# Optimization experiments

Hardware: AMD Instinct MI355X
Metric: run time of the kernel (lower is better)

## Reference

```python
import jax, jax.numpy as jnp
import numpy as np

B, S, D, H = 4, 2048, 1024, 16
HD = D // H  # head_dim = 64


def setup_inputs() -> dict:
    key = jax.random.key(0)
    k1, k2, k3 = jax.random.split(key, 3)
    x = jax.random.normal(k1, (B, S, D), dtype=jnp.float32)
    W_attn = jax.random.normal(k2, (D, 3 * D), dtype=jnp.float32) * (1.0 / np.sqrt(D))
    b_attn = jnp.zeros((3 * D,), dtype=jnp.float32)
    W_proj = jax.random.normal(k3, (D, D), dtype=jnp.float32) * (1.0 / np.sqrt(D))
    b_proj = jnp.zeros((D,), dtype=jnp.float32)
    return {"x": x, "W_attn": W_attn, "b_attn": b_attn, "W_proj": W_proj, "b_proj": b_proj}


def reference(x, W_attn, b_attn, W_proj, b_proj):
    bsz, seq_len, d = x.shape
    n_head = H
    head_dim = d // n_head
    qkv = x @ W_attn + b_attn                      # [B,S,3D]
    q, k, v = jnp.split(qkv, 3, axis=-1)           # each [B,S,D]
    # -> [B,H,S,hd]
    q = q.reshape(bsz, seq_len, n_head, head_dim).transpose(0, 2, 1, 3)
    k = k.reshape(bsz, seq_len, n_head, head_dim).transpose(0, 2, 1, 3)
    v = v.reshape(bsz, seq_len, n_head, head_dim).transpose(0, 2, 1, 3)
    scale = 1.0 / np.sqrt(head_dim).astype(np.float32)
    att = jnp.einsum("bhqd,bhkd->bhqk", q, k) * scale  # [B,H,S,S]
    causal = jnp.tril(jnp.ones((seq_len, seq_len), dtype=bool))
    att = jnp.where(causal[None, None], att, jnp.float32(-jnp.inf))
    att = jax.nn.softmax(att, axis=-1)
    y = jnp.einsum("bhqk,bhkd->bhqd", att, v)       # [B,H,S,hd]
    y = y.transpose(0, 2, 1, 3).reshape(bsz, seq_len, d)
    return y @ W_proj + b_proj
```

## Files before the change

kernel.cpp:

```cpp
#include <hip/hip_runtime.h>

typedef __attribute__((ext_vector_type(8))) short short8;
typedef __attribute__((ext_vector_type(8))) __bf16 bf16x8;
typedef __attribute__((ext_vector_type(2))) __bf16 bf16x2;
typedef __attribute__((ext_vector_type(4))) float f32x4;
typedef __attribute__((ext_vector_type(2))) unsigned int uint2v;

#define LOG2E 1.44269504088896340736f

__device__ __forceinline__ unsigned short f2b(float f) {
  unsigned u = __builtin_bit_cast(unsigned, f);
  u += 0x7fffu + ((u >> 16) & 1u);
  return (unsigned short)(u >> 16);
}
__device__ __forceinline__ float b2f(unsigned short s) {
  unsigned u = (unsigned)s << 16;
  return __builtin_bit_cast(float, u);
}
__device__ __forceinline__ bf16x8 asbf(short8 s) { return __builtin_bit_cast(bf16x8, s); }

__device__ __forceinline__ void gl_lds16(const void* g, void* l) {
  __builtin_amdgcn_global_load_lds(
      (const __attribute__((address_space(1))) void*)g,
      (__attribute__((address_space(3))) void*)l, 16, 0, 0);
}

__device__ __forceinline__ unsigned lds_a(const void* p) {
  return (unsigned)(size_t)(__attribute__((address_space(3))) const void*)p;
}

__device__ __forceinline__ unsigned pk_bf16(float a, float b) {
  bf16x2 v;
  v[0] = (__bf16)a;
  v[1] = (__bf16)b;
  return __builtin_bit_cast(unsigned, v);
}

__global__ void k_cvt_bf16(const float* __restrict__ x, unsigned short* __restrict__ o, int n) {
  int i = (blockIdx.x * 256 + threadIdx.x) * 4;
  if (i >= n) return;
  float4 v = *(const float4*)(x + i);
  ushort4 r;
  r.x = f2b(v.x); r.y = f2b(v.y); r.z = f2b(v.z); r.w = f2b(v.w);
  *(ushort4*)(o + i) = r;
}

__global__ void k_transpose_bf16(const float* __restrict__ W, unsigned short* __restrict__ Wt,
                                 int R, int C) {
  __shared__ float tile[64][65];
  const int tc = blockIdx.x, tr = blockIdx.y;
  const int r0 = tr * 64, c0 = tc * 64;
  for (int it = 0; it < 16; ++it) {
    int lin = it * 256 + threadIdx.x;
    int r = lin >> 6, c = lin & 63;
    tile[r][c] = W[(size_t)(r0 + r) * C + c0 + c];
  }
  __syncthreads();
  for (int it = 0; it < 16; ++it) {
    int lin = it * 256 + threadIdx.x;
    int orr = lin >> 6, oc = lin & 63;
    Wt[(size_t)(c0 + orr) * R + r0 + oc] = f2b(tile[oc][orr]);
  }
}

template <int BNW, bool OUT_BF16>
__global__ __launch_bounds__(512, 4)
void k_gemm256(const unsigned short* __restrict__ A, const unsigned short* __restrict__ Bt,
               const float* __restrict__ bias, void* __restrict__ Cp,
               int M, int N, int K) {
  constexpr int BN = BNW * 4;
  constexpr int NR = BNW / 16;
  __shared__ unsigned short lds[2][512 * 32];

  const int tid = threadIdx.x;
  const int wv = tid >> 6, lane = tid & 63;
  const int g = lane >> 4, l15 = lane & 15;
  const int wr = wv >> 2, wc = wv & 3;

  const int ntn = N / BN;
  const int nwg = gridDim.x;
  const int bid = blockIdx.x;
  const int cpx = nwg >> 3;
  const int swz = (bid & 7) * cpx + (bid >> 3);
  const int tm = swz / ntn, tn = swz % ntn;

  const unsigned short* Ab = A + (size_t)(tm * 256) * K;
  const unsigned short* Bb = Bt + (size_t)(tn * BN) * K;

  const int NT = K >> 5;

  auto As = [&](int buf) -> char* { return (char*)&lds[buf][0]; };
  auto Bs = [&](int buf) -> char* { return (char*)&lds[buf][256 * 32]; };

  auto stageA = [&](int buf, int t) {
#pragma unroll
    for (int it = 0; it < 2; ++it) {
      int cidx = it * 512 + tid;
      int row = cidx >> 2, c8 = cidx & 3;
      int sc = c8 ^ ((row >> 1) & 3);
      gl_lds16(Ab + (size_t)row * K + t * 32 + sc * 8, As(buf) + cidx * 16);
    }
  };
  auto stageB = [&](int buf, int t) {
#pragma unroll
    for (int it = 0; it < 2; ++it) {
      int cidx = it * 512 + tid;
      int row = cidx >> 2, c8 = cidx & 3;
      int sc = c8 ^ ((row >> 1) & 3);
      int grow = (row < BN) ? row : 0;
      gl_lds16(Bb + (size_t)grow * K + t * 32 + sc * 8, Bs(buf) + cidx * 16);
    }
  };

  auto rdA = [&](int buf, int ms) -> short8 {
    int row = wr * 128 + ms * 16 + l15;
    int ch = g ^ ((row >> 1) & 3);
    return *(const short8*)(As(buf) + row * 64 + ch * 16);
  };
  auto rdB = [&](int buf, int n) -> short8 {
    int row = wc * BNW + n * 16 + l15;
    int ch = g ^ ((row >> 1) & 3);
    return *(const short8*)(Bs(buf) + row * 64 + ch * 16);
  };

  f32x4 acc[8][NR] = {};

  stageA(0, 0);
  stageB(0, 0);
  stageB(1, 1);
  asm volatile("s_waitcnt vmcnt(2)" ::: "memory");
  __builtin_amdgcn_s_barrier();

  for (int t = 0; t < NT; ++t) {
    const int buf = t & 1, nbuf = buf ^ 1;
    short8 bfr[NR], a0, a1;

    if (t + 1 < NT) stageA(nbuf, t + 1);
#pragma unroll
    for (int n = 0; n < NR; ++n) bfr[n] = rdB(buf, n);
    a0 = rdA(buf, 0);
    a1 = rdA(buf, 1);
    asm volatile("s_waitcnt lgkmcnt(0)" ::: "memory");
    __builtin_amdgcn_sched_barrier(0);
    __builtin_amdgcn_s_barrier();
    __builtin_amdgcn_s_setprio(1);
#pragma unroll
    for (int n = 0; n < NR; ++n) {
      acc[0][n] = __builtin_amdgcn_mfma_f32_16x16x32_bf16(asbf(a0), asbf(bfr[n]), acc[0][n], 0, 0, 0);
      acc[1][n] = __builtin_amdgcn_mfma_f32_16x16x32_bf16(asbf(a1), asbf(bfr[n]), acc[1][n], 0, 0, 0);
    }
    a0 = rdA(buf, 2);
    a1 = rdA(buf, 3);
#pragma unroll
    for (int n = 0; n < NR; ++n) {
      acc[2][n] = __builtin_amdgcn_mfma_f32_16x16x32_bf16(asbf(a0), asbf(bfr[n]), acc[2][n], 0, 0, 0);
      acc[3][n] = __builtin_amdgcn_mfma_f32_16x16x32_bf16(asbf(a1), asbf(bfr[n]), acc[3][n], 0, 0, 0);
    }
    __builtin_amdgcn_s_setprio(0);

    if (t + 2 < NT) stageB(buf, t + 2);
    a0 = rdA(buf, 4);
    a1 = rdA(buf, 5);
    asm volatile("s_waitcnt lgkmcnt(0)" ::: "memory");
    __builtin_amdgcn_sched_barrier(0);
    __builtin_amdgcn_s_barrier();
    __builtin_amdgcn_s_setprio(1);
#pragma unroll
    for (int n = 0; n < NR; ++n) {
      acc[4][n] = __builtin_amdgcn_mfma_f32_16x16x32_bf16(asbf(a0), asbf(bfr[n]), acc[4][n], 0, 0, 0);
      acc[5][n] = __builtin_amdgcn_mfma_f32_16x16x32_bf16(asbf(a1), asbf(bfr[n]), acc[5][n], 0, 0, 0);
    }
    a0 = rdA(buf, 6);
    a1 = rdA(buf, 7);
#pragma unroll
    for (int n = 0; n < NR; ++n) {
      acc[6][n] = __builtin_amdgcn_mfma_f32_16x16x32_bf16(asbf(a0), asbf(bfr[n]), acc[6][n], 0, 0, 0);
      acc[7][n] = __builtin_amdgcn_mfma_f32_16x16x32_bf16(asbf(a1), asbf(bfr[n]), acc[7][n], 0, 0, 0);
    }
    __builtin_amdgcn_s_setprio(0);
    if (t + 2 < NT) asm volatile("s_waitcnt vmcnt(2)" ::: "memory");
    else            asm volatile("s_waitcnt vmcnt(0)" ::: "memory");
    __builtin_amdgcn_s_barrier();
  }

  const int crow0 = tm * 256 + wr * 128 + g * 4;
  const int ccol0 = tn * BN + wc * BNW + l15;
#pragma unroll
  for (int n = 0; n < NR; ++n) {
    int col = ccol0 + n * 16;
    float bv = bias[col];
#pragma unroll
    for (int mq = 0; mq < 8; ++mq)
#pragma unroll
      for (int j = 0; j < 4; ++j) {
        int row = crow0 + mq * 16 + j;
        float v = acc[mq][n][j] + bv;
        if constexpr (OUT_BF16)
          ((unsigned short*)Cp)[(size_t)row * N + col] = f2b(v);
        else
          ((float*)Cp)[(size_t)row * N + col] = v;
      }
  }
}

__global__ __launch_bounds__(512)
void k_attn(const unsigned short* __restrict__ qkv, unsigned short* __restrict__ y) {
  constexpr int SEQ = 2048, TD = 3072, DM = 1024;
  __shared__ unsigned short Kl[2][4096];
  __shared__ unsigned short Vl[2][4096];
  __shared__ unsigned short Pl[8][2048];

  const int f = blockIdx.x;
  const int wrk = (f & 7) * 32 + (f >> 3);
  const int bh = wrk >> 2, pr = wrk & 3;
  const int b = bh >> 4, h = bh & 15;
  const int tid = threadIdx.x;
  const int lane = tid & 63, w = tid >> 6;
  const int g = lane >> 4, l15 = lane & 15;

  const size_t base = (size_t)b * SEQ * TD + h * 64;
  const unsigned short* Kg0 = qkv + base + 1024;
  const unsigned short* Vg0 = qkv + base + 2048;

  short8 onesb;
#pragma unroll
  for (int i = 0; i < 8; ++i) onesb[i] = (short)0x3F80;

  auto stage = [&](int buf, int c) {
    const unsigned short* Kg = Kg0 + (size_t)(c * 64) * TD;
    const unsigned short* Vg = Vg0 + (size_t)(c * 64) * TD;
    const int j = tid;
    int r = j >> 3, cc = j & 7;
    int cck = cc ^ (r & 7);
    gl_lds16(Kg + (size_t)r * TD + cck * 8, (char*)Kl[buf] + j * 16);
    int kv = ((j >> 1) & 3) | (((j >> 5) & 1) << 2) | (((j >> 3) & 3) << 3) |
             (((j >> 6) & 1) << 5);
    int d0 = ((j >> 7) << 4) | ((j & 1) << 3);
    gl_lds16(Vg + (size_t)kv * TD + d0, (char*)Vl[buf] + j * 16);
  };

  char* pw = (char*)Pl + w * 4096;

  for (int half = 0; half < 2; ++half) {
    const int qt = half ? (7 - pr) : pr;
    const int q0 = qt * 256;
    const int qw = w * 32;

    short8 qf[2][2];
#pragma unroll
    for (int qg = 0; qg < 2; ++qg) {
      const unsigned short* qrow = qkv + base + (size_t)(q0 + qw + qg * 16 + l15) * TD;
#pragma unroll
      for (int kh = 0; kh < 2; ++kh) {
        short8 t = *(const short8*)(qrow + kh * 32 + g * 8);
#pragma unroll
        for (int i = 0; i < 8; ++i)
          t[i] = (short)f2b(b2f((unsigned short)t[i]) * (0.125f * LOG2E));
        qf[qg][kh] = t;
      }
    }

    f32x4 o[2][4] = {};
    f32x4 ol[2] = {};

    const int nch = 4 * (qt + 1);
    int cur = 0;
    stage(0, 0);
    for (int c = 0; c < nch; ++c) {
      if (c + 1 < nch) {
        stage(cur ^ 1, c + 1);
        asm volatile("s_waitcnt vmcnt(2)" ::: "memory");
      } else {
        asm volatile("s_waitcnt vmcnt(0)" ::: "memory");
      }
      __builtin_amdgcn_s_barrier();

      f32x4 sv[2][4];
      __builtin_amdgcn_s_setprio(1);
#pragma unroll
      for (int ff = 0; ff < 4; ++ff) {
        int kv = ff * 16 + l15;
        short8 kf0 = *(const short8*)((const char*)Kl[cur] + kv * 128 + ((g) ^ (kv & 7)) * 16);
        short8 kf1 = *(const short8*)((const char*)Kl[cur] + kv * 128 + ((4 + g) ^ (kv & 7)) * 16);
#pragma unroll
        for (int qg = 0; qg < 2; ++qg) {
          f32x4 s = {};
          s = __builtin_amdgcn_mfma_f32_16x16x32_bf16(asbf(kf0), asbf(qf[qg][0]), s, 0, 0, 0);
          s = __builtin_amdgcn_mfma_f32_16x16x32_bf16(asbf(kf1), asbf(qf[qg][1]), s, 0, 0, 0);
          sv[qg][ff] = s;
        }
      }
      __builtin_amdgcn_s_setprio(0);

      const int crel = c - 4 * qt;
      if (crel >= 0) {
#pragma unroll
        for (int qg = 0; qg < 2; ++qg)
#pragma unroll
          for (int ff = 0; ff < 4; ++ff)
#pragma unroll
            for (int r = 0; r < 4; ++r)
              if (crel * 64 + ff * 16 + g * 4 + r > qw + qg * 16 + l15)
                sv[qg][ff][r] = -128.f;
      }

#pragma unroll
      for (int qg = 0; qg < 2; ++qg)
#pragma unroll
        for (int ff = 0; ff < 4; ++ff) {
          float p0 = __builtin_amdgcn_exp2f(sv[qg][ff][0]);
          float p1 = __builtin_amdgcn_exp2f(sv[qg][ff][1]);
          float p2 = __builtin_amdgcn_exp2f(sv[qg][ff][2]);
          float p3 = __builtin_amdgcn_exp2f(sv[qg][ff][3]);
          unsigned w0 = pk_bf16(p0, p1);
          unsigned w1 = pk_bf16(p2, p3);
          unsigned long long pk = (unsigned long long)w0 | ((unsigned long long)w1 << 32);
          int off = qg * 2048 + ((l15 * 128 + ff * 32 + g * 8) ^ ((l15 & 7) << 4));
          *(unsigned long long*)(pw + off) = pk;
        }

      const unsigned vaddr = lds_a((const char*)Vl[cur] + g * 128 + l15 * 8);
#pragma unroll
      for (int kvh = 0; kvh < 2; ++kvh) {
        uint2v t0[4], t1[4];
#pragma unroll
        for (int n = 0; n < 4; ++n) {
          asm volatile("ds_read_b64_tr_b16 %0, %1 offset:%2"
                       : "=v"(t0[n]) : "v"(vaddr), "i"(n * 2048 + kvh * 1024));
          asm volatile("ds_read_b64_tr_b16 %0, %1 offset:%2"
                       : "=v"(t1[n]) : "v"(vaddr), "i"(n * 2048 + kvh * 1024 + 512));
        }
        asm volatile("s_waitcnt lgkmcnt(0)" ::: "memory");
        __builtin_amdgcn_sched_barrier(0);
        __builtin_amdgcn_s_setprio(1);
#pragma unroll
        for (int qg = 0; qg < 2; ++qg) {
          short8 pa = *(const short8*)(pw + qg * 2048 +
                                       ((l15 * 128 + kvh * 64 + g * 16) ^ ((l15 & 7) << 4)));
#pragma unroll
          for (int n = 0; n < 4; ++n) {
            union { uint2v u[2]; short8 s; } uu;
            uu.u[0] = t0[n]; uu.u[1] = t1[n];
            o[qg][n] = __builtin_amdgcn_mfma_f32_16x16x32_bf16(asbf(pa), asbf(uu.s),
                                                               o[qg][n], 0, 0, 0);
          }
          ol[qg] = __builtin_amdgcn_mfma_f32_16x16x32_bf16(asbf(pa), asbf(onesb),
                                                           ol[qg], 0, 0, 0);
        }
        __builtin_amdgcn_s_setprio(0);
      }

      __builtin_amdgcn_s_barrier();
      cur ^= 1;
    }

#pragma unroll
    for (int qg = 0; qg < 2; ++qg) {
      float lj[4];
#pragma unroll
      for (int j = 0; j < 4; ++j) lj[j] = 1.f / ol[qg][j];
#pragma unroll
      for (int n = 0; n < 4; ++n)
#pragma unroll
        for (int j = 0; j < 4; ++j) {
          int row = q0 + qw + qg * 16 + g * 4 + j;
          int col = h * 64 + n * 16 + l15;
          y[(size_t)(b * SEQ + row) * DM + col] = f2b(o[qg][n][j] * lj[j]);
        }
    }
  }
}

extern "C" void kernel_launch(void* const* d_in, const int* in_sizes, int n_in,
                              void* d_out, int out_size, void* d_ws, size_t ws_size,
                              hipStream_t stream) {
  const float* x = (const float*)d_in[0];
  const float* W_attn = (const float*)d_in[1];
  const float* b_attn = (const float*)d_in[2];
  const float* W_proj = (const float*)d_in[3];
  const float* b_proj = (const float*)d_in[4];
  float* out = (float*)d_out;

  const int B = 4, S = 2048, D = 1024;
  const int M = B * S;
  const int TD = 3 * D;

  char* ws = (char*)d_ws;
  unsigned short* qkvb = (unsigned short*)ws;
  unsigned short* xb = (unsigned short*)(ws + (size_t)M * TD * 2);
  unsigned short* Wat = (unsigned short*)(ws + (size_t)M * TD * 2 + (size_t)M * D * 2);
  unsigned short* Wpt = Wat + (size_t)TD * D;

  k_cvt_bf16<<<(M * D) / 1024, 256, 0, stream>>>(x, xb, M * D);
  k_transpose_bf16<<<dim3(TD / 64, D / 64), 256, 0, stream>>>(W_attn, Wat, D, TD);
  k_transpose_bf16<<<dim3(D / 64, D / 64), 256, 0, stream>>>(W_proj, Wpt, D, D);

  k_gemm256<48, true><<<(M / 256) * (TD / 192), 512, 0, stream>>>(xb, Wat, b_attn, qkvb, M, TD, D);
  k_attn<<<256, 512, 0, stream>>>(qkvb, xb);
  k_gemm256<32, false><<<(M / 256) * (D / 128), 512, 0, stream>>>(xb, Wpt, b_proj, out, M, D, D);
}
```

Before: 191.2 us.

## Fuse prep kernels, unify GEMM to 256x128 tiles, double attention KV chunk

Merges the x-to-bf16 conversion and both weight transposes into one prep launch, which removes two kernel launches. Replaces the templated GEMM with a single 256x128 tile variant for both projections, so the QKV GEMM moves from 192-wide to 128-wide N tiles and one B load per stage. Doubles the attention KV chunk from 64 to 128 keys, which halves the number of barriers and staging rounds per query tile at the cost of twice the LDS use and more registers for scores. The smaller QKV tile raises the block count but reduces reuse per block, and the larger LDS footprint may lower attention occupancy.

```diff
diff --git a/kernel.cpp b/kernel.cpp
--- a/kernel.cpp
+++ b/kernel.cpp
@@ -36,44 +36,65 @@
   return __builtin_bit_cast(unsigned, v);
 }
 
-__global__ void k_cvt_bf16(const float* __restrict__ x, unsigned short* __restrict__ o, int n) {
-  int i = (blockIdx.x * 256 + threadIdx.x) * 4;
-  if (i >= n) return;
-  float4 v = *(const float4*)(x + i);
-  ushort4 r;
-  r.x = f2b(v.x); r.y = f2b(v.y); r.z = f2b(v.z); r.w = f2b(v.w);
-  *(ushort4*)(o + i) = r;
-}
-
-__global__ void k_transpose_bf16(const float* __restrict__ W, unsigned short* __restrict__ Wt,
-                                 int R, int C) {
+template <int N>
+__device__ __forceinline__ void wait_vm() {
+  if constexpr (N == 4) asm volatile("s_waitcnt vmcnt(4)" ::: "memory");
+  else if constexpr (N == 1) asm volatile("s_waitcnt vmcnt(1)" ::: "memory");
+  else asm volatile("s_waitcnt vmcnt(0)" ::: "memory");
+}
+
+__device__ __forceinline__ void transpose_tile(const float* __restrict__ W,
+                                               unsigned short* __restrict__ Wt,
+                                               int R, int C, int tc, int tr, int tid) {
   __shared__ float tile[64][65];
-  const int tc = blockIdx.x, tr = blockIdx.y;
   const int r0 = tr * 64, c0 = tc * 64;
   for (int it = 0; it < 16; ++it) {
-    int lin = it * 256 + threadIdx.x;
+    int lin = it * 256 + tid;
     int r = lin >> 6, c = lin & 63;
     tile[r][c] = W[(size_t)(r0 + r) * C + c0 + c];
   }
   __syncthreads();
   for (int it = 0; it < 16; ++it) {
-    int lin = it * 256 + threadIdx.x;
+    int lin = it * 256 + tid;
     int orr = lin >> 6, oc = lin & 63;
     Wt[(size_t)(c0 + orr) * R + r0 + oc] = f2b(tile[oc][orr]);
   }
 }
 
-template <int BNW, bool OUT_BF16>
-__global__ __launch_bounds__(512, 4)
-void k_gemm256(const unsigned short* __restrict__ A, const unsigned short* __restrict__ Bt,
-               const float* __restrict__ bias, void* __restrict__ Cp,
-               int M, int N, int K) {
-  constexpr int BN = BNW * 4;
-  constexpr int NR = BNW / 16;
-  __shared__ unsigned short lds[2][512 * 32];
+__global__ __launch_bounds__(256)
+void k_prep(const float* __restrict__ x, unsigned short* __restrict__ xb,
+            const float* __restrict__ Wa, unsigned short* __restrict__ Wat,
+            const float* __restrict__ Wp, unsigned short* __restrict__ Wpt) {
+  const int bid = blockIdx.x, tid = threadIdx.x;
+  if (bid < 2048) {
+    size_t i = ((size_t)bid * 256 + tid) * 16;
+#pragma unroll
+    for (int v = 0; v < 4; ++v) {
+      float4 f = *(const float4*)(x + i + v * 4);
+      ushort4 r;
+      r.x = f2b(f.x); r.y = f2b(f.y); r.z = f2b(f.z); r.w = f2b(f.w);
+      *(ushort4*)(xb + i + v * 4) = r;
+    }
+  } else if (bid < 2816) {
+    int idx = bid - 2048;
+    transpose_tile(Wa, Wat, 1024, 3072, idx % 48, idx / 48, tid);
+  } else {
+    int idx = bid - 2816;
+    transpose_tile(Wp, Wpt, 1024, 1024, idx % 16, idx / 16, tid);
+  }
+}
+
+template <bool OUT_BF16>
+__global__ __launch_bounds__(512)
+void k_gemm_bk32(const unsigned short* __restrict__ A, const unsigned short* __restrict__ Bt,
+                 const float* __restrict__ bias, void* __restrict__ Cp,
+                 int M, int N, int K) {
+  constexpr int BNW = 32, NR = 2, BN = 128;
+  __shared__ unsigned short lds[2][384 * 32];
 
   const int tid = threadIdx.x;
-  const int wv = tid >> 6, lane = tid & 63;
+  const int lane = tid & 63;
+  const int wv = tid >> 6;
   const int g = lane >> 4, l15 = lane & 15;
   const int wr = wv >> 2, wc = wv & 3;
 
@@ -102,14 +123,10 @@
     }
   };
   auto stageB = [&](int buf, int t) {
-#pragma unroll
-    for (int it = 0; it < 2; ++it) {
-      int cidx = it * 512 + tid;
-      int row = cidx >> 2, c8 = cidx & 3;
-      int sc = c8 ^ ((row >> 1) & 3);
-      int grow = (row < BN) ? row : 0;
-      gl_lds16(Bb + (size_t)grow * K + t * 32 + sc * 8, Bs(buf) + cidx * 16);
-    }
+    int cidx = tid;
+    int row = cidx >> 2, c8 = cidx & 3;
+    int sc = c8 ^ ((row >> 1) & 3);
+    gl_lds16(Bb + (size_t)row * K + t * 32 + sc * 8, Bs(buf) + cidx * 16);
   };
 
   auto rdA = [&](int buf, int ms) -> short8 {
@@ -128,7 +145,7 @@
   stageA(0, 0);
   stageB(0, 0);
   stageB(1, 1);
-  asm volatile("s_waitcnt vmcnt(2)" ::: "memory");
+  wait_vm<1>();
   __builtin_amdgcn_s_barrier();
 
   for (int t = 0; t < NT; ++t) {
@@ -178,8 +195,8 @@
       acc[7][n] = __builtin_amdgcn_mfma_f32_16x16x32_bf16(asbf(a1), asbf(bfr[n]), acc[7][n], 0, 0, 0);
     }
     __builtin_amdgcn_s_setprio(0);
-    if (t + 2 < NT) asm volatile("s_waitcnt vmcnt(2)" ::: "memory");
-    else            asm volatile("s_waitcnt vmcnt(0)" ::: "memory");
+    if (t + 2 < NT) wait_vm<1>();
+    else            wait_vm<0>();
     __builtin_amdgcn_s_barrier();
   }
 
@@ -206,9 +223,9 @@
 __global__ __launch_bounds__(512)
 void k_attn(const unsigned short* __restrict__ qkv, unsigned short* __restrict__ y) {
   constexpr int SEQ = 2048, TD = 3072, DM = 1024;
-  __shared__ unsigned short Kl[2][4096];
-  __shared__ unsigned short Vl[2][4096];
-  __shared__ unsigned short Pl[8][2048];
+  __shared__ unsigned short Kl[2][8192];
+  __shared__ unsigned short Vl[2][8192];
+  __shared__ unsigned short Pl[8][4096];
 
   const int f = blockIdx.x;
   const int wrk = (f & 7) * 32 + (f >> 3);
@@ -227,19 +244,22 @@
   for (int i = 0; i < 8; ++i) onesb[i] = (short)0x3F80;
 
   auto stage = [&](int buf, int c) {
-    const unsigned short* Kg = Kg0 + (size_t)(c * 64) * TD;
-    const unsigned short* Vg = Vg0 + (size_t)(c * 64) * TD;
-    const int j = tid;
-    int r = j >> 3, cc = j & 7;
-    int cck = cc ^ (r & 7);
-    gl_lds16(Kg + (size_t)r * TD + cck * 8, (char*)Kl[buf] + j * 16);
-    int kv = ((j >> 1) & 3) | (((j >> 5) & 1) << 2) | (((j >> 3) & 3) << 3) |
-             (((j >> 6) & 1) << 5);
-    int d0 = ((j >> 7) << 4) | ((j & 1) << 3);
-    gl_lds16(Vg + (size_t)kv * TD + d0, (char*)Vl[buf] + j * 16);
+    const unsigned short* Kg = Kg0 + (size_t)(c * 128) * TD;
+    const unsigned short* Vg = Vg0 + (size_t)(c * 128) * TD;
+#pragma unroll
+    for (int it = 0; it < 2; ++it) {
+      int j = it * 512 + tid;
+      int r = j >> 3, cc = j & 7;
+      int cck = cc ^ (r & 7);
+      gl_lds16(Kg + (size_t)r * TD + cck * 8, (char*)Kl[buf] + j * 16);
+      int kv = ((j >> 1) & 3) | (((j >> 5) & 1) << 2) | (((j >> 3) & 3) << 3) |
+               (((j >> 6) & 1) << 5) | ((j >> 9) << 6);
+      int d0 = (((j >> 7) & 3) << 4) | ((j & 1) << 3);
+      gl_lds16(Vg + (size_t)kv * TD + d0, (char*)Vl[buf] + j * 16);
+    }
   };
 
-  char* pw = (char*)Pl + w * 4096;
+  char* pw = (char*)Pl + w * 8192;
 
   for (int half = 0; half < 2; ++half) {
     const int qt = half ? (7 - pr) : pr;
@@ -263,22 +283,22 @@
     f32x4 o[2][4] = {};
     f32x4 ol[2] = {};
 
-    const int nch = 4 * (qt + 1);
+    const int nch = 2 * (qt + 1);
     int cur = 0;
     stage(0, 0);
     for (int c = 0; c < nch; ++c) {
       if (c + 1 < nch) {
         stage(cur ^ 1, c + 1);
-        asm volatile("s_waitcnt vmcnt(2)" ::: "memory");
+        wait_vm<4>();
       } else {
-        asm volatile("s_waitcnt vmcnt(0)" ::: "memory");
+        wait_vm<0>();
       }
       __builtin_amdgcn_s_barrier();
 
-      f32x4 sv[2][4];
+      f32x4 sv[2][8];
       __builtin_amdgcn_s_setprio(1);
 #pragma unroll
-      for (int ff = 0; ff < 4; ++ff) {
+      for (int ff = 0; ff < 8; ++ff) {
         int kv = ff * 16 + l15;
         short8 kf0 = *(const short8*)((const char*)Kl[cur] + kv * 128 + ((g) ^ (kv & 7)) * 16);
         short8 kf1 = *(const short8*)((const char*)Kl[cur] + kv * 128 + ((4 + g) ^ (kv & 7)) * 16);
@@ -292,22 +312,22 @@
       }
       __builtin_amdgcn_s_setprio(0);
 
-      const int crel = c - 4 * qt;
+      const int crel = c - 2 * qt;
       if (crel >= 0) {
 #pragma unroll
         for (int qg = 0; qg < 2; ++qg)
 #pragma unroll
-          for (int ff = 0; ff < 4; ++ff)
+          for (int ff = 0; ff < 8; ++ff)
 #pragma unroll
             for (int r = 0; r < 4; ++r)
-              if (crel * 64 + ff * 16 + g * 4 + r > qw + qg * 16 + l15)
+              if (crel * 128 + ff * 16 + g * 4 + r > qw + qg * 16 + l15)
                 sv[qg][ff][r] = -128.f;
       }
 
 #pragma unroll
       for (int qg = 0; qg < 2; ++qg)
 #pragma unroll
-        for (int ff = 0; ff < 4; ++ff) {
+        for (int ff = 0; ff < 8; ++ff) {
           float p0 = __builtin_amdgcn_exp2f(sv[qg][ff][0]);
           float p1 = __builtin_amdgcn_exp2f(sv[qg][ff][1]);
           float p2 = __builtin_amdgcn_exp2f(sv[qg][ff][2]);
@@ -315,28 +335,30 @@
           unsigned w0 = pk_bf16(p0, p1);
           unsigned w1 = pk_bf16(p2, p3);
           unsigned long long pk = (unsigned long long)w0 | ((unsigned long long)w1 << 32);
-          int off = qg * 2048 + ((l15 * 128 + ff * 32 + g * 8) ^ ((l15 & 7) << 4));
+          int off = (ff >> 2) * 4096 + qg * 2048 +
+                    ((l15 * 128 + (ff & 3) * 32 + g * 8) ^ ((l15 & 7) << 4));
           *(unsigned long long*)(pw + off) = pk;
         }
 
       const unsigned vaddr = lds_a((const char*)Vl[cur] + g * 128 + l15 * 8);
 #pragma unroll
-      for (int kvh = 0; kvh < 2; ++kvh) {
+      for (int kvh = 0; kvh < 4; ++kvh) {
+        const int sub = kvh >> 1, kvl = kvh & 1;
         uint2v t0[4], t1[4];
 #pragma unroll
         for (int n = 0; n < 4; ++n) {
           asm volatile("ds_read_b64_tr_b16 %0, %1 offset:%2"
-                       : "=v"(t0[n]) : "v"(vaddr), "i"(n * 2048 + kvh * 1024));
+                       : "=v"(t0[n]) : "v"(vaddr), "i"(sub * 8192 + n * 2048 + kvl * 1024));
           asm volatile("ds_read_b64_tr_b16 %0, %1 offset:%2"
-                       : "=v"(t1[n]) : "v"(vaddr), "i"(n * 2048 + kvh * 1024 + 512));
+                       : "=v"(t1[n]) : "v"(vaddr), "i"(sub * 8192 + n * 2048 + kvl * 1024 + 512));
         }
         asm volatile("s_waitcnt lgkmcnt(0)" ::: "memory");
         __builtin_amdgcn_sched_barrier(0);
         __builtin_amdgcn_s_setprio(1);
 #pragma unroll
         for (int qg = 0; qg < 2; ++qg) {
-          short8 pa = *(const short8*)(pw + qg * 2048 +
-                                       ((l15 * 128 + kvh * 64 + g * 16) ^ ((l15 & 7) << 4)));
+          short8 pa = *(const short8*)(pw + sub * 4096 + qg * 2048 +
+                                       ((l15 * 128 + kvl * 64 + g * 16) ^ ((l15 & 7) << 4)));
 #pragma unroll
           for (int n = 0; n < 4; ++n) {
             union { uint2v u[2]; short8 s; } uu;
@@ -391,11 +413,8 @@
   unsigned short* Wat = (unsigned short*)(ws + (size_t)M * TD * 2 + (size_t)M * D * 2);
   unsigned short* Wpt = Wat + (size_t)TD * D;
 
-  k_cvt_bf16<<<(M * D) / 1024, 256, 0, stream>>>(x, xb, M * D);
-  k_transpose_bf16<<<dim3(TD / 64, D / 64), 256, 0, stream>>>(W_attn, Wat, D, TD);
-  k_transpose_bf16<<<dim3(D / 64, D / 64), 256, 0, stream>>>(W_proj, Wpt, D, D);
-
-  k_gemm256<48, true><<<(M / 256) * (TD / 192), 512, 0, stream>>>(xb, Wat, b_attn, qkvb, M, TD, D);
+  k_prep<<<3072, 256, 0, stream>>>(x, xb, W_attn, Wat, W_proj, Wpt);
+  k_gemm_bk32<true><<<(M / 256) * (TD / 128), 512, 0, stream>>>(xb, Wat, b_attn, qkvb, M, TD, D);
   k_attn<<<256, 512, 0, stream>>>(qkvb, xb);
-  k_gemm256<32, false><<<(M / 256) * (D / 128), 512, 0, stream>>>(xb, Wpt, b_proj, out, M, D, D);
-}
+  k_gemm_bk32<false><<<(M / 256) * (D / 128), 512, 0, stream>>>(xb, Wpt, b_proj, out, M, D, D);
+}
```

New measurement: 161.8 us (median of 2 runs). 15.4% less time.
